# Kernel optimization log

Measured on AMD Instinct MI355X. Metric: run time of the kernel, lower is better.

Reference implementation:

```python
import jax, jax.numpy as jnp
import numpy as np

D_MODEL = 512

def setup_inputs() -> dict:
    key = jax.random.key(0)
    k1, k2, k3, k4, k5 = jax.random.split(key, 5)
    x = jax.random.normal(k1, (8, D_MODEL, 2048), dtype=jnp.float32)
    s = 1.0 / np.sqrt(D_MODEL)
    W_qkv = jax.random.uniform(k2, (D_MODEL, 3 * D_MODEL), dtype=jnp.float32, minval=-s, maxval=s)
    b_qkv = jax.random.uniform(k3, (3 * D_MODEL,), dtype=jnp.float32, minval=-s, maxval=s)
    W_proj = jax.random.uniform(k4, (D_MODEL, D_MODEL), dtype=jnp.float32, minval=-s, maxval=s)
    b_proj = jax.random.uniform(k5, (D_MODEL,), dtype=jnp.float32, minval=-s, maxval=s)
    return {"x": x, "W_qkv": W_qkv, "b_qkv": b_qkv, "W_proj": W_proj, "b_proj": b_proj}

def reference(x, W_qkv, b_qkv, W_proj, b_proj):
    # x: [B, L, N] with L == d_model; attend across the N variable axis
    xt = jnp.swapaxes(x, 1, 2)                      # [B, N, L]
    L = xt.shape[-1]
    qkv = xt @ W_qkv + b_qkv                        # [B, N, 3L]
    q, k, v = jnp.split(qkv, 3, axis=-1)            # each [B, N, L]
    attn = jnp.einsum('bnd,bmd->bnm', q, k) / jnp.sqrt(jnp.float32(L))
    attn = jax.nn.softmax(attn, axis=-1)            # [B, N, N]
    out = jnp.einsum('bnm,bmd->bnd', attn, v)       # [B, N, L]
    out = out @ W_proj + b_proj                     # [B, N, L]
    return jnp.swapaxes(out, 1, 2)                  # [B, L, N]
```

## Files before the change

### kernel.cpp

```cpp
#include <hip/hip_runtime.h>

#define NVAR 2048
#define DM   512
#define J3   1536

typedef _Float16 f16;
typedef _Float16 f16x8 __attribute__((ext_vector_type(8)));
typedef _Float16 f16x4 __attribute__((ext_vector_type(4)));
typedef float    f32x4 __attribute__((ext_vector_type(4)));

#define SBAR() do { asm volatile("s_barrier" ::: "memory"); \
                    __builtin_amdgcn_sched_barrier(0); } while(0)
#define LGKM0() do { asm volatile("s_waitcnt lgkmcnt(0)" ::: "memory"); \
                     __builtin_amdgcn_sched_barrier(0); } while(0)
#define GLOAD(gp, lp) __builtin_amdgcn_global_load_lds( \
    (const __attribute__((address_space(1))) void*)(gp), \
    (__attribute__((address_space(3))) void*)(lp), 16, 0, 0)

__device__ __forceinline__ void waitvm_n(int n) {
    switch (n) {
    case 0: asm volatile("s_waitcnt vmcnt(0)" ::: "memory"); break;
    case 1: asm volatile("s_waitcnt vmcnt(1)" ::: "memory"); break;
    case 2: asm volatile("s_waitcnt vmcnt(2)" ::: "memory"); break;
    case 3: asm volatile("s_waitcnt vmcnt(3)" ::: "memory"); break;
    case 4: asm volatile("s_waitcnt vmcnt(4)" ::: "memory"); break;
    case 5: asm volatile("s_waitcnt vmcnt(5)" ::: "memory"); break;
    case 6: asm volatile("s_waitcnt vmcnt(6)" ::: "memory"); break;
    case 7: asm volatile("s_waitcnt vmcnt(7)" ::: "memory"); break;
    case 8: asm volatile("s_waitcnt vmcnt(8)" ::: "memory"); break;
    default: break;
    }
    __builtin_amdgcn_sched_barrier(0);
}

__global__ __launch_bounds__(256)
void k_tr(const float* __restrict__ src, f16* __restrict__ dst,
          int R, int C, long bsSrc, long bsDst) {
    __shared__ float t[64][65];
    const float* s = src + (size_t)blockIdx.z * bsSrc;
    f16* d = dst + (size_t)blockIdx.z * bsDst;
    const int c0 = blockIdx.x * 64, r0 = blockIdx.y * 64;
    const int lx = threadIdx.x & 15, ly = threadIdx.x >> 4;
#pragma unroll
    for (int p = 0; p < 4; ++p) {
        int r = p * 16 + ly;
        f32x4 v = *(const f32x4*)(s + (size_t)(r0 + r) * C + c0 + lx * 4);
#pragma unroll
        for (int i = 0; i < 4; ++i) t[r][lx * 4 + i] = v[i];
    }
    __syncthreads();
#pragma unroll
    for (int p = 0; p < 4; ++p) {
        int c = p * 16 + ly;
        f16x4 h;
#pragma unroll
        for (int i = 0; i < 4; ++i) h[i] = (f16)t[lx * 4 + i][c];
        *(f16x4*)(d + (size_t)(c0 + c) * R + r0 + lx * 4) = h;
    }
}

__global__ __launch_bounds__(256)
void k_cast(const float* __restrict__ W, f16* __restrict__ out) {
    int idx = blockIdx.x * 256 + threadIdx.x;
    int gi = idx * 4;
    int d = gi >> 9, j = gi & 511;
    f32x4 v = *(const f32x4*)(W + (size_t)d * J3 + 1024 + j);
    f16x4 h;
#pragma unroll
    for (int i = 0; i < 4; ++i) h[i] = (f16)v[i];
    *(f16x4*)(out + (size_t)d * 512 + j) = h;
}

__global__ __launch_bounds__(512)
void k_bvp(const float* __restrict__ bqkv, const float* __restrict__ Wp,
           float* __restrict__ bias_c) {
    const int l = threadIdx.x;
    float a[8] = {};
    for (int j = 0; j < 512; j += 8)
#pragma unroll
        for (int u = 0; u < 8; ++u)
            a[u] += bqkv[1024 + j + u] * Wp[(size_t)(j + u) * DM + l];
    float s = ((a[0] + a[1]) + (a[2] + a[3])) + ((a[4] + a[5]) + (a[6] + a[7]));
    bias_c[1024 + l] = s;
    bias_c[l] = bqkv[l];
    bias_c[512 + l] = bqkv[512 + l];
}

#define ASZ (256 * 64)
__global__ __launch_bounds__(512, 2)
void gemm_sp(const f16* __restrict__ A, const f16* __restrict__ B,
             long bsA, long bsB, int lda, int ldb, int K,
             float scale, f16* __restrict__ o0) {
    __shared__ f16 smem[5 * ASZ];
    f16* sA = smem;
    f16* sB = smem + 3 * ASZ;

    const int tid  = threadIdx.x;
    const int lane = tid & 63;
    const int w    = __builtin_amdgcn_readfirstlane(tid >> 6);
    const int wm   = (w >> 2) * 128;
    const int wn   = (w & 3) * 64;
    const int z    = blockIdx.x;
    const int bid  = blockIdx.y;
    const int bxA  = bid & 7;
    const int bxB  = bid >> 3;

    const f16* Ab = A + (size_t)z * bsA + (size_t)bxA * 256 * lda;
    const f16* Bb = B + (size_t)z * bsB + (size_t)bxB * 256 * ldb;

    int offA[2][2], offB[2][2];
#pragma unroll
    for (int h = 0; h < 2; ++h)
#pragma unroll
        for (int i = 0; i < 2; ++i) {
            int slot = i * 512 + tid;
            int row  = h * 128 + (slot >> 3);
            int s    = (slot & 7) ^ (row & 7);
            offA[h][i] = row * lda + s * 8;
            offB[h][i] = row * ldb + s * 8;
        }

    auto STG_A = [&](int kt, int h, int buf) {
        f16* d = sA + buf * ASZ + h * 8192;
#pragma unroll
        for (int i = 0; i < 2; ++i)
            GLOAD(Ab + offA[h][i] + kt * 64, d + (i * 512 + tid) * 8);
    };
    auto STG_B = [&](int kt, int h, int buf) {
        f16* d = sB + buf * ASZ + h * 8192;
#pragma unroll
        for (int i = 0; i < 2; ++i)
            GLOAD(Bb + offB[h][i] + kt * 64, d + (i * 512 + tid) * 8);
    };

    int koff[2];
#pragma unroll
    for (int ks = 0; ks < 2; ++ks)
        koff[ks] = ((ks * 4 + (lane >> 4)) ^ (lane & 7)) * 8;
    const int rowA = (wm + (lane & 15)) * 64;
    const int rowB = (wn + (lane & 15)) * 64;

    f16x8 av[8][2], bv[4][2];
    f32x4 acc[8][4] = {};

    auto LD_AV = [&](const f16* p, int mi0) {
#pragma unroll
        for (int mi = 0; mi < 4; ++mi)
#pragma unroll
            for (int ks = 0; ks < 2; ++ks)
                av[mi0 + mi][ks] = *(const f16x8*)(p + rowA + (mi0 + mi) * 1024 + koff[ks]);
    };
    auto LD_BV = [&](const f16* p, int nj0) {
#pragma unroll
        for (int nj = 0; nj < 2; ++nj)
#pragma unroll
            for (int ks = 0; ks < 2; ++ks)
                bv[nj0 + nj][ks] = *(const f16x8*)(p + rowB + (nj0 + nj) * 1024 + koff[ks]);
    };
    auto MM = [&](int mi0, int nj0) {
        __builtin_amdgcn_s_setprio(1);
#pragma unroll
        for (int mi = 0; mi < 4; ++mi)
#pragma unroll
            for (int nj = 0; nj < 2; ++nj)
#pragma unroll
                for (int ks = 0; ks < 2; ++ks)
                    acc[mi0 + mi][nj0 + nj] = __builtin_amdgcn_mfma_f32_16x16x32_f16(
                        av[mi0 + mi][ks], bv[nj0 + nj][ks], acc[mi0 + mi][nj0 + nj], 0, 0, 0);
        __builtin_amdgcn_s_setprio(0);
    };

    const int NT = K >> 6;
    int issued = 0, markB = 0;

    STG_A(0, 0, 0); STG_A(0, 1, 0); issued += 4;
    STG_B(0, 0, 0); STG_B(0, 1, 0); issued += 4; markB = issued;
    if (NT > 1) { STG_A(1, 0, 1); STG_A(1, 1, 1); issued += 4; }
    waitvm_n(issued - markB);
    SBAR();

    int iA = 0, iB = 0;
    for (int t = 0; t < NT; ++t) {
        const f16* pA = sA + iA * ASZ;
        const f16* pB = sB + iB * ASZ;
        const int bufB2 = iB ^ 1;
        int bufA2 = iA + 2; if (bufA2 >= 3) bufA2 -= 3;

        LD_BV(pB, 0); LD_AV(pA, 0);
        if (t + 1 < NT) { STG_B(t + 1, 0, bufB2); issued += 2; }
        SBAR(); LGKM0();
        MM(0, 0);
        SBAR();

        LD_BV(pB, 2);
        if (t + 1 < NT) { STG_B(t + 1, 1, bufB2); issued += 2; markB = issued; }
        SBAR(); LGKM0();
        MM(0, 2);
        SBAR();

        LD_AV(pA, 4);
        if (t + 2 < NT) { STG_A(t + 2, 0, bufA2); issued += 2; }
        SBAR(); LGKM0();
        MM(4, 2);
        SBAR();

        if (t + 2 < NT) { STG_A(t + 2, 1, bufA2); issued += 2; }
        if (t + 1 < NT) { waitvm_n(issued - markB); SBAR(); }
        MM(4, 0);
        if (t + 1 < NT) SBAR();

        iA = (iA + 1 == 3) ? 0 : iA + 1;
        iB ^= 1;
    }

    const int rb0 = bxA * 256 + wm + (lane >> 4) * 4;
    const int cb0 = bxB * 256 + wn + (lane & 15);
#pragma unroll
    for (int mi = 0; mi < 8; ++mi)
#pragma unroll
        for (int nj = 0; nj < 4; ++nj) {
            f16x4 vv;
#pragma unroll
            for (int r = 0; r < 4; ++r)
                vv[r] = (f16)__expf(acc[mi][nj][r] * scale);
            *(f16x4*)(o0 + ((size_t)z * NVAR + cb0 + nj * 16) * NVAR
                           + rb0 + mi * 16) = vv;
        }
}

#define BSZO (128 * 64)
__global__ __launch_bounds__(512, 2)
void gemm_out(const f16* __restrict__ A, const f16* __restrict__ B,
              long bsA, long bsB, int lda, int ldb, int K,
              const float* __restrict__ bias, float* __restrict__ of) {
    __shared__ f16 smem[3 * ASZ + 2 * BSZO];
    f16* sA = smem;
    f16* sB = smem + 3 * ASZ;

    const int tid  = threadIdx.x;
    const int lane = tid & 63;
    const int w    = __builtin_amdgcn_readfirstlane(tid >> 6);
    const int wm   = (w >> 1) * 64;
    const int wn   = (w & 1) * 64;
    const int z    = blockIdx.x;
    const int bid  = blockIdx.y;
    const int bxA  = bid & 7;
    const int bxB  = bid >> 3;

    const f16* Ab = A + (size_t)z * bsA + (size_t)bxA * 256 * lda;
    const f16* Bb = B + (size_t)z * bsB + (size_t)bxB * 128 * ldb;

    int offA[2][2], offB[2];
#pragma unroll
    for (int h = 0; h < 2; ++h)
#pragma unroll
        for (int i = 0; i < 2; ++i) {
            int slot = i * 512 + tid;
            int row  = h * 128 + (slot >> 3);
            int s    = (slot & 7) ^ (row & 7);
            offA[h][i] = row * lda + s * 8;
        }
#pragma unroll
    for (int h = 0; h < 2; ++h) {
        int row = h * 64 + (tid >> 3);
        int s   = (tid & 7) ^ (row & 7);
        offB[h] = row * ldb + s * 8;
    }

    auto STG_A = [&](int kt, int buf) {
        f16* d = sA + buf * ASZ;
#pragma unroll
        for (int h = 0; h < 2; ++h)
#pragma unroll
            for (int i = 0; i < 2; ++i)
                GLOAD(Ab + offA[h][i] + kt * 64, d + h * 8192 + (i * 512 + tid) * 8);
    };
    auto STG_B = [&](int kt, int buf) {
        f16* d = sB + buf * BSZO;
#pragma unroll
        for (int h = 0; h < 2; ++h)
            GLOAD(Bb + offB[h] + kt * 64, d + h * 4096 + tid * 8);
    };

    int koff[2];
#pragma unroll
    for (int ks = 0; ks < 2; ++ks)
        koff[ks] = ((ks * 4 + (lane >> 4)) ^ (lane & 7)) * 8;
    const int rowA = (wm + (lane & 15)) * 64;
    const int rowB = (wn + (lane & 15)) * 64;

    f16x8 ones;
#pragma unroll
    for (int e = 0; e < 8; ++e) ones[e] = (f16)1.0f;

    f16x8 av[4][2], bv[4][2];
    f32x4 acc[4][4] = {};
    f32x4 accrs[4] = {};

    auto LD_AV = [&](const f16* p, int mi0) {
#pragma unroll
        for (int mi = 0; mi < 2; ++mi)
#pragma unroll
            for (int ks = 0; ks < 2; ++ks)
                av[mi0 + mi][ks] = *(const f16x8*)(p + rowA + (mi0 + mi) * 1024 + koff[ks]);
    };
    auto LD_BV = [&](const f16* p) {
#pragma unroll
        for (int nj = 0; nj < 4; ++nj)
#pragma unroll
            for (int ks = 0; ks < 2; ++ks)
                bv[nj][ks] = *(const f16x8*)(p + rowB + nj * 1024 + koff[ks]);
    };
    auto MM = [&](int mi0) {
        __builtin_amdgcn_s_setprio(1);
#pragma unroll
        for (int mi = 0; mi < 2; ++mi)
#pragma unroll
            for (int ks = 0; ks < 2; ++ks) {
                accrs[mi0 + mi] = __builtin_amdgcn_mfma_f32_16x16x32_f16(
                    av[mi0 + mi][ks], ones, accrs[mi0 + mi], 0, 0, 0);
#pragma unroll
                for (int nj = 0; nj < 4; ++nj)
                    acc[mi0 + mi][nj] = __builtin_amdgcn_mfma_f32_16x16x32_f16(
                        av[mi0 + mi][ks], bv[nj][ks], acc[mi0 + mi][nj], 0, 0, 0);
            }
        __builtin_amdgcn_s_setprio(0);
    };

    const int NT = K >> 6;
    int issued = 0, markB = 0;

    STG_A(0, 0); issued += 4;
    STG_B(0, 0); issued += 2; markB = issued;
    if (NT > 1) { STG_A(1, 1); issued += 4; }
    waitvm_n(issued - markB);
    SBAR();

    int iA = 0, iB = 0;
    for (int t = 0; t < NT; ++t) {
        const f16* pA = sA + iA * ASZ;
        const f16* pB = sB + iB * BSZO;
        int bufA2 = iA + 2; if (bufA2 >= 3) bufA2 -= 3;

        LD_BV(pB); LD_AV(pA, 0);
        if (t + 1 < NT) { STG_B(t + 1, iB ^ 1); issued += 2; markB = issued; }
        SBAR(); LGKM0();
        MM(0);
        SBAR();

        LD_AV(pA, 2);
        if (t + 2 < NT) { STG_A(t + 2, bufA2); issued += 4; }
        SBAR(); LGKM0();
        MM(2);
        if (t + 1 < NT) { waitvm_n(issued - markB); SBAR(); }

        iA = (iA + 1 == 3) ? 0 : iA + 1;
        iB ^= 1;
    }

    const int rb0 = bxA * 256 + wm + (lane >> 4) * 4;
    const int cb0 = bxB * 128 + wn + (lane & 15);
#pragma unroll
    for (int mi = 0; mi < 4; ++mi) {
        f32x4 inv;
#pragma unroll
        for (int r = 0; r < 4; ++r) inv[r] = 1.0f / accrs[mi][r];
#pragma unroll
        for (int nj = 0; nj < 4; ++nj) {
            const int l = cb0 + nj * 16;
            const float bb = bias[l];
            f32x4 vv;
#pragma unroll
            for (int r = 0; r < 4; ++r) vv[r] = acc[mi][nj][r] * inv[r] + bb;
            *(f32x4*)(of + ((size_t)z * DM + l) * NVAR + rb0 + mi * 16) = vv;
        }
    }
}

template<int MODE>
__global__ __launch_bounds__(256)
void gemm_f16(const f16* __restrict__ A, const f16* __restrict__ B,
              long bsA, long bsB, int lda, int ldb, int K, int nbx,
              const float* __restrict__ bias,
              f16* __restrict__ o0, f16* __restrict__ o1, f16* __restrict__ o2) {
    __shared__ f16 sA[128 * 64];
    __shared__ f16 sB[128 * 64];
    const int tid  = threadIdx.x;
    const int lane = tid & 63;
    const int w    = __builtin_amdgcn_readfirstlane(tid >> 6);
    const int wm   = (w >> 1) * 64;
    const int wn   = (w & 1) * 64;
    const int z    = blockIdx.x;
    const int bid  = blockIdx.y;
    const int bxA  = bid % nbx;
    const int bxB  = bid / nbx;

    const f16* Ab = A + (size_t)z * bsA + (size_t)bxA * 128 * lda;
    const f16* Bb = B + (size_t)z * bsB + (size_t)bxB * 128 * ldb;

    int srcA[4], srcB[4];
#pragma unroll
    for (int i = 0; i < 4; ++i) {
        int slot = i * 256 + tid;
        int row  = slot >> 3;
        int s    = (slot & 7) ^ (row & 7);
        srcA[i] = row * lda + s * 8;
        srcB[i] = row * ldb + s * 8;
    }

    f32x4 acc[4][4] = {};

    for (int k0 = 0; k0 < K; k0 += 64) {
        __syncthreads();
#pragma unroll
        for (int i = 0; i < 4; ++i) {
            GLOAD(Ab + srcA[i] + k0, sA + i * 2048 + w * 512);
            GLOAD(Bb + srcB[i] + k0, sB + i * 2048 + w * 512);
        }
        __syncthreads();
#pragma unroll
        for (int kh = 0; kh < 2; ++kh) {
            f16x8 av[4], bv[4];
#pragma unroll
            for (int mi = 0; mi < 4; ++mi) {
                int r = wm + mi * 16 + (lane & 15);
                int s = (kh * 4 + (lane >> 4)) ^ (r & 7);
                av[mi] = *(const f16x8*)(sA + r * 64 + s * 8);
            }
#pragma unroll
            for (int nj = 0; nj < 4; ++nj) {
                int r = wn + nj * 16 + (lane & 15);
                int s = (kh * 4 + (lane >> 4)) ^ (r & 7);
                bv[nj] = *(const f16x8*)(sB + r * 64 + s * 8);
            }
#pragma unroll
            for (int mi = 0; mi < 4; ++mi)
#pragma unroll
                for (int nj = 0; nj < 4; ++nj)
                    acc[mi][nj] = __builtin_amdgcn_mfma_f32_16x16x32_f16(
                        av[mi], bv[nj], acc[mi][nj], 0, 0, 0);
        }
    }

    const int rb0 = bxA * 128 + wm + (lane >> 4) * 4;
    const int cb0 = bxB * 128 + wn + (lane & 15);

    if (MODE == 0) {
        const int seg = (bxA * 128) >> 9;
#pragma unroll
        for (int mi = 0; mi < 4; ++mi) {
            const int j = rb0 + mi * 16;
            const f32x4 b4 = *(const f32x4*)(bias + j);
#pragma unroll
            for (int nj = 0; nj < 4; ++nj) {
                const int n = cb0 + nj * 16;
                if (seg == 2) {
#pragma unroll
                    for (int r = 0; r < 4; ++r)
                        o2[((size_t)z * DM + (j - 1024 + r)) * NVAR + n] =
                            (f16)(acc[mi][nj][r] + b4[r]);
                } else {
                    f16* dst = seg ? o1 : o0;
                    const int jj = seg ? j - 512 : j;
                    f16x4 vv;
#pragma unroll
                    for (int r = 0; r < 4; ++r) vv[r] = (f16)(acc[mi][nj][r] + b4[r]);
                    *(f16x4*)(dst + ((size_t)z * NVAR + n) * DM + jj) = vv;
                }
            }
        }
    } else {
#pragma unroll
        for (int mi = 0; mi < 4; ++mi)
#pragma unroll
            for (int nj = 0; nj < 4; ++nj) {
                f16x4 vv;
#pragma unroll
                for (int r = 0; r < 4; ++r) vv[r] = (f16)acc[mi][nj][r];
                *(f16x4*)(o0 + ((size_t)(cb0 + nj * 16)) * DM
                               + rb0 + mi * 16) = vv;
            }
    }
}

extern "C" void kernel_launch(void* const* d_in, const int* in_sizes, int n_in,
                              void* d_out, int out_size, void* d_ws, size_t ws_size,
                              hipStream_t stream) {
    const float* x     = (const float*)d_in[0];
    const float* Wqkv  = (const float*)d_in[1];
    const float* bqkv  = (const float*)d_in[2];
    const float* Wproj = (const float*)d_in[3];
    const float* bproj = (const float*)d_in[4];
    float* out = (float*)d_out;

    const size_t PB = (size_t)NVAR * DM;
    f16* xT   = (f16*)d_ws;
    f16* q    = xT + 8 * PB;
    f16* kk   = q  + 8 * PB;
    f16* vwT  = kk + 8 * PB;
    f16* S    = vwT + 8 * PB;
    f16* scr  = S  + (size_t)8 * NVAR * NVAR;
    f16* WqT  = scr + 8 * PB;
    f16* WpT  = WqT + (size_t)J3 * DM;
    f16* Wq2  = scr;
    float* bias_c = (float*)(scr + 512 * 512);

    k_tr<<<dim3(NVAR / 64, DM / 64, 8), 256, 0, stream>>>(
        x, xT, DM, NVAR, (long)DM * NVAR, (long)NVAR * DM);
    k_tr<<<dim3(16, DM / 64, 1), 256, 0, stream>>>(Wqkv, WqT, DM, J3, 0, 0);
    k_tr<<<dim3(DM / 64, DM / 64, 1), 256, 0, stream>>>(Wproj, WpT, DM, DM, 0, 0);
    k_cast<<<dim3(256), 256, 0, stream>>>(Wqkv, Wq2);
    k_bvp<<<dim3(1), 512, 0, stream>>>(bqkv, Wproj, bias_c);

    gemm_f16<4><<<dim3(1, 16), 256, 0, stream>>>(
        Wq2, WpT, 0, 0, 512, DM, DM, 4,
        nullptr, WqT + (size_t)1024 * DM, nullptr, nullptr);

    gemm_f16<0><<<dim3(8, 12 * 16), 256, 0, stream>>>(
        WqT, xT, 0, (long)NVAR * DM, DM, DM, DM, 12,
        bias_c, q, kk, vwT);

    gemm_sp<<<dim3(8, 8 * 8), 512, 0, stream>>>(
        kk, q, (long)NVAR * DM, (long)NVAR * DM, DM, DM, DM,
        0.044194173824159216f, S);

    gemm_out<<<dim3(8, 32), 512, 0, stream>>>(
        S, vwT, (long)NVAR * NVAR, (long)DM * NVAR, NVAR, NVAR, NVAR,
        bproj, out);
}
```

Before: 187.6 us.

## Stage score tile through LDS for coalesced stores; retile output GEMM; parallelize bias

The score GEMM epilogue now writes exp'd fp16 values into swizzled shared memory and then stores full contiguous 16-byte rows to global memory, instead of scattered 8-byte column-strided writes. The output GEMM is retiled from 256x128 to 128x256 blocks (A tile 128 rows, B tile 256 rows) with a 2x4 warp layout, changing the load balance between the S and V operands. The bias-projection kernel is split across 8 blocks with a shared-memory reduction instead of a single block. The goal is better global write coalescing and less serial overhead, at the cost of extra LDS traffic and a barrier in the epilogue.

After: 173.6 us (median of 3 runs). -7.5%, faster.

```diff
diff --git a/kernel.cpp b/kernel.cpp
--- a/kernel.cpp
+++ b/kernel.cpp
@@ -71,19 +71,24 @@
     *(f16x4*)(out + (size_t)d * 512 + j) = h;
 }
 
-__global__ __launch_bounds__(512)
+__global__ __launch_bounds__(256)
 void k_bvp(const float* __restrict__ bqkv, const float* __restrict__ Wp,
            float* __restrict__ bias_c) {
-    const int l = threadIdx.x;
-    float a[8] = {};
-    for (int j = 0; j < 512; j += 8)
-#pragma unroll
-        for (int u = 0; u < 8; ++u)
-            a[u] += bqkv[1024 + j + u] * Wp[(size_t)(j + u) * DM + l];
-    float s = ((a[0] + a[1]) + (a[2] + a[3])) + ((a[4] + a[5]) + (a[6] + a[7]));
-    bias_c[1024 + l] = s;
-    bias_c[l] = bqkv[l];
-    bias_c[512 + l] = bqkv[512 + l];
+    const int b = blockIdx.x;
+    const int lt = threadIdx.x & 63, js = threadIdx.x >> 6;
+    const int l = b * 64 + lt;
+    float s = 0.f;
+    for (int j = js * 128; j < js * 128 + 128; ++j)
+        s += bqkv[1024 + j] * Wp[(size_t)j * DM + l];
+    __shared__ float red[4][64];
+    red[js][lt] = s;
+    __syncthreads();
+    if (js == 0)
+        bias_c[1024 + l] = (red[0][lt] + red[1][lt]) + (red[2][lt] + red[3][lt]);
+    if (threadIdx.x < 128) {
+        int i = b * 128 + threadIdx.x;
+        bias_c[i] = bqkv[i];
+    }
 }
 
 #define ASZ (256 * 64)
@@ -213,73 +218,85 @@
         iB ^= 1;
     }
 
-    const int rb0 = bxA * 256 + wm + (lane >> 4) * 4;
-    const int cb0 = bxB * 256 + wn + (lane & 15);
-#pragma unroll
-    for (int mi = 0; mi < 8; ++mi)
+    const int n0 = bxB * 256;
+    const int m0 = bxA * 256;
+    f16* bb = smem;
+#pragma unroll
+    for (int mi = 0; mi < 8; ++mi) {
+        const int m    = wm + mi * 16 + ((lane >> 4) << 2);
+        const int c16  = m >> 3;
+        const int half = m & 4;
 #pragma unroll
         for (int nj = 0; nj < 4; ++nj) {
+            const int nl = wn + nj * 16 + (lane & 15);
             f16x4 vv;
 #pragma unroll
             for (int r = 0; r < 4; ++r)
                 vv[r] = (f16)__expf(acc[mi][nj][r] * scale);
-            *(f16x4*)(o0 + ((size_t)z * NVAR + cb0 + nj * 16) * NVAR
-                           + rb0 + mi * 16) = vv;
+            *(f16x4*)(bb + nl * 256 + ((c16 ^ (nl & 7)) << 3) + half) = vv;
         }
-}
-
-#define BSZO (128 * 64)
+    }
+    LGKM0();
+    SBAR();
+#pragma unroll
+    for (int it = 0; it < 16; ++it) {
+        const int row = it * 16 + (tid >> 5);
+        const int ch  = tid & 31;
+        f16x8 v = *(const f16x8*)(bb + row * 256 + ((ch ^ (row & 7)) << 3));
+        *(f16x8*)(o0 + ((size_t)z * NVAR + n0 + row) * NVAR + m0 + ch * 8) = v;
+    }
+}
+
+#define AO (128 * 64)
+#define BO (256 * 64)
 __global__ __launch_bounds__(512, 2)
 void gemm_out(const f16* __restrict__ A, const f16* __restrict__ B,
               long bsA, long bsB, int lda, int ldb, int K,
               const float* __restrict__ bias, float* __restrict__ of) {
-    __shared__ f16 smem[3 * ASZ + 2 * BSZO];
+    __shared__ f16 smem[3 * AO + 2 * BO];
     f16* sA = smem;
-    f16* sB = smem + 3 * ASZ;
+    f16* sB = smem + 3 * AO;
 
     const int tid  = threadIdx.x;
     const int lane = tid & 63;
     const int w    = __builtin_amdgcn_readfirstlane(tid >> 6);
-    const int wm   = (w >> 1) * 64;
-    const int wn   = (w & 1) * 64;
+    const int wm   = (w >> 2) * 64;
+    const int wn   = (w & 3) * 64;
     const int z    = blockIdx.x;
     const int bid  = blockIdx.y;
-    const int bxA  = bid & 7;
-    const int bxB  = bid >> 3;
-
-    const f16* Ab = A + (size_t)z * bsA + (size_t)bxA * 256 * lda;
-    const f16* Bb = B + (size_t)z * bsB + (size_t)bxB * 128 * ldb;
-
-    int offA[2][2], offB[2];
-#pragma unroll
-    for (int h = 0; h < 2; ++h)
-#pragma unroll
-        for (int i = 0; i < 2; ++i) {
-            int slot = i * 512 + tid;
-            int row  = h * 128 + (slot >> 3);
-            int s    = (slot & 7) ^ (row & 7);
-            offA[h][i] = row * lda + s * 8;
-        }
-#pragma unroll
-    for (int h = 0; h < 2; ++h) {
-        int row = h * 64 + (tid >> 3);
-        int s   = (tid & 7) ^ (row & 7);
-        offB[h] = row * ldb + s * 8;
+    const int bxA  = bid & 15;
+    const int bxB  = bid >> 4;
+
+    const f16* Ab = A + (size_t)z * bsA + (size_t)bxA * 128 * lda;
+    const f16* Bb = B + (size_t)z * bsB + (size_t)bxB * 256 * ldb;
+
+    int offA[2], offB[4];
+#pragma unroll
+    for (int i = 0; i < 2; ++i) {
+        int slot = i * 512 + tid;
+        int row  = slot >> 3;
+        int s    = (slot & 7) ^ (row & 7);
+        offA[i] = row * lda + s * 8;
+    }
+#pragma unroll
+    for (int i = 0; i < 4; ++i) {
+        int slot = i * 512 + tid;
+        int row  = slot >> 3;
+        int s    = (slot & 7) ^ (row & 7);
+        offB[i] = row * ldb + s * 8;
     }
 
     auto STG_A = [&](int kt, int buf) {
-        f16* d = sA + buf * ASZ;
-#pragma unroll
-        for (int h = 0; h < 2; ++h)
-#pragma unroll
-            for (int i = 0; i < 2; ++i)
-                GLOAD(Ab + offA[h][i] + kt * 64, d + h * 8192 + (i * 512 + tid) * 8);
+        f16* d = sA + buf * AO;
+#pragma unroll
+        for (int i = 0; i < 2; ++i)
+            GLOAD(Ab + offA[i] + kt * 64, d + (i * 512 + tid) * 8);
     };
     auto STG_B = [&](int kt, int buf) {
-        f16* d = sB + buf * BSZO;
-#pragma unroll
-        for (int h = 0; h < 2; ++h)
-            GLOAD(Bb + offB[h] + kt * 64, d + h * 4096 + tid * 8);
+        f16* d = sB + buf * BO;
+#pragma unroll
+        for (int i = 0; i < 4; ++i)
+            GLOAD(Bb + offB[i] + kt * 64, d + (i * 512 + tid) * 8);
     };
 
     int koff[2];
@@ -330,26 +347,26 @@
     const int NT = K >> 6;
     int issued = 0, markB = 0;
 
-    STG_A(0, 0); issued += 4;
-    STG_B(0, 0); issued += 2; markB = issued;
-    if (NT > 1) { STG_A(1, 1); issued += 4; }
+    STG_A(0, 0); issued += 2;
+    STG_B(0, 0); issued += 4; markB = issued;
+    if (NT > 1) { STG_A(1, 1); issued += 2; }
     waitvm_n(issued - markB);
     SBAR();
 
     int iA = 0, iB = 0;
     for (int t = 0; t < NT; ++t) {
-        const f16* pA = sA + iA * ASZ;
-        const f16* pB = sB + iB * BSZO;
+        const f16* pA = sA + iA * AO;
+        const f16* pB = sB + iB * BO;
         int bufA2 = iA + 2; if (bufA2 >= 3) bufA2 -= 3;
 
         LD_BV(pB); LD_AV(pA, 0);
-        if (t + 1 < NT) { STG_B(t + 1, iB ^ 1); issued += 2; markB = issued; }
+        if (t + 1 < NT) { STG_B(t + 1, iB ^ 1); issued += 4; markB = issued; }
         SBAR(); LGKM0();
         MM(0);
         SBAR();
 
         LD_AV(pA, 2);
-        if (t + 2 < NT) { STG_A(t + 2, bufA2); issued += 4; }
+        if (t + 2 < NT) { STG_A(t + 2, bufA2); issued += 2; }
         SBAR(); LGKM0();
         MM(2);
         if (t + 1 < NT) { waitvm_n(issued - markB); SBAR(); }
@@ -358,8 +375,8 @@
         iB ^= 1;
     }
 
-    const int rb0 = bxA * 256 + wm + (lane >> 4) * 4;
-    const int cb0 = bxB * 128 + wn + (lane & 15);
+    const int rb0 = bxA * 128 + wm + (lane >> 4) * 4;
+    const int cb0 = bxB * 256 + wn + (lane & 15);
 #pragma unroll
     for (int mi = 0; mi < 4; ++mi) {
         f32x4 inv;
@@ -510,7 +527,7 @@
     k_tr<<<dim3(16, DM / 64, 1), 256, 0, stream>>>(Wqkv, WqT, DM, J3, 0, 0);
     k_tr<<<dim3(DM / 64, DM / 64, 1), 256, 0, stream>>>(Wproj, WpT, DM, DM, 0, 0);
     k_cast<<<dim3(256), 256, 0, stream>>>(Wqkv, Wq2);
-    k_bvp<<<dim3(1), 512, 0, stream>>>(bqkv, Wproj, bias_c);
+    k_bvp<<<dim3(8), 256, 0, stream>>>(bqkv, Wproj, bias_c);
 
     gemm_f16<4><<<dim3(1, 16), 256, 0, stream>>>(
         Wq2, WpT, 0, 0, 512, DM, DM, 4,
```
